# Kernel tuning notes

Hardware: AMD Instinct MI355X
Metric: run time of the kernel (lower is better)

The kernel has to match this reference:

```python
import jax, jax.numpy as jnp
import numpy as np

BINS = 10


def setup_inputs() -> dict:
    key = jax.random.key(0)
    k1, k2 = jax.random.split(key)
    N, C = 4194304, 16
    inputs = jax.random.normal(k1, (N, C), dtype=jnp.float32)
    target = jax.random.randint(k2, (N,), 0, 2, dtype=jnp.int64)
    return {"inputs": inputs, "target": target}


def reference(inputs, target):
    N = inputs.shape[0]
    edges = jnp.arange(BINS + 1, dtype=inputs.dtype) / BINS  # [0, 0.1, ..., 1.0]

    # p_t = softmax(inputs)[i, target_i]
    logp = jax.nn.log_softmax(inputs, axis=1)
    p_t = jnp.take_along_axis(jnp.exp(logp), target[:, None], axis=1)[:, 0]

    # gradient norm g = |p_t - target| (detached in the original)
    g = jnp.abs(jax.lax.stop_gradient(p_t) - target.astype(inputs.dtype))

    # bin index: matches (g >= edges[i]) & (g < edges[i+1]); clip handles g == 1.0
    bin_idx = jnp.clip(jnp.searchsorted(edges, g, side="right") - 1, 0, BINS - 1)

    # per-bin counts via one scatter-add (replaces the per-bin CPU loop)
    counts = jax.ops.segment_sum(jnp.ones_like(g), bin_idx, num_segments=BINS)
    counts = jnp.maximum(counts, 1.0)  # occupied bins always have count >= 1

    # weights[i] = (N / bins) / num_in_bin(i)
    weights = (N / BINS) / counts[bin_idx]

    # weighted cross entropy, summed
    nll = -jnp.take_along_axis(logp, target[:, None], axis=1)[:, 0]
    return jnp.sum(nll * weights)
```

## Files before the change

kernel.cpp:

```cpp
#include <hip/hip_runtime.h>

#define BINS 10

__global__ __launch_bounds__(256) void ghm_main(const float* __restrict__ x,
                                                const int* __restrict__ tgt,
                                                double* __restrict__ g_sum,
                                                unsigned int* __restrict__ g_cnt,
                                                int n_rows) {
    __shared__ double s_sum[BINS];
    __shared__ unsigned int s_cnt[BINS];
    if (threadIdx.x < BINS) { s_sum[threadIdx.x] = 0.0; s_cnt[threadIdx.x] = 0u; }
    __syncthreads();

    const int j = threadIdx.x & 3;
    const int quad = (blockIdx.x * blockDim.x + threadIdx.x) >> 2;
    const int quads_total = (gridDim.x * blockDim.x) >> 2;

    const float edges[BINS + 1] = {0.0f, 0.1f, 0.2f, 0.3f, 0.4f, 0.5f,
                                   0.6f, 0.7f, 0.8f, 0.9f, 1.0f};

    for (int row = quad; row < n_rows; row += quads_total) {
        const float4 v = ((const float4*)x)[row * 4 + j];

        float m = fmaxf(fmaxf(v.x, v.y), fmaxf(v.z, v.w));
        m = fmaxf(m, __shfl_xor(m, 1));
        m = fmaxf(m, __shfl_xor(m, 2));

        float s = expf(v.x - m) + expf(v.y - m) + expf(v.z - m) + expf(v.w - m);
        s += __shfl_xor(s, 1);
        s += __shfl_xor(s, 2);

        if (j == 0) {
            const int t = tgt[row];
            const float xt = (t == 0) ? v.x : ((t == 1) ? v.y : ((t == 2) ? v.z : v.w));
            const float logp = xt - m - logf(s);
            const float p = expf(logp);
            const float g = fabsf(p - (float)t);

            int b = 0;
            #pragma unroll
            for (int k = 1; k <= BINS; ++k) b += (g >= edges[k]) ? 1 : 0;
            if (b > BINS - 1) b = BINS - 1;

            atomicAdd(&s_cnt[b], 1u);
            atomicAdd(&s_sum[b], (double)(-logp));
        }
    }
    __syncthreads();

    if (threadIdx.x < BINS) {
        if (s_cnt[threadIdx.x] != 0u) {
            atomicAdd(&g_cnt[threadIdx.x], s_cnt[threadIdx.x]);
            atomicAdd(&g_sum[threadIdx.x], s_sum[threadIdx.x]);
        }
    }
}

__global__ void ghm_final(const double* __restrict__ g_sum,
                          const unsigned int* __restrict__ g_cnt,
                          float* __restrict__ out, int n_rows) {
    if (threadIdx.x == 0 && blockIdx.x == 0) {
        const double scale = (double)n_rows / (double)BINS;
        double total = 0.0;
        for (int b = 0; b < BINS; ++b) {
            double c = (double)g_cnt[b];
            if (c < 1.0) c = 1.0;
            total += g_sum[b] / c;
        }
        out[0] = (float)(total * scale);
    }
}

extern "C" void kernel_launch(void* const* d_in, const int* in_sizes, int n_in,
                              void* d_out, int out_size, void* d_ws, size_t ws_size,
                              hipStream_t stream) {
    const float* x = (const float*)d_in[0];
    const int* tgt = (const int*)d_in[1];
    const int n_rows = in_sizes[1];

    double* g_sum = (double*)d_ws;
    unsigned int* g_cnt = (unsigned int*)((char*)d_ws + BINS * sizeof(double));

    hipMemsetAsync(d_ws, 0, BINS * (sizeof(double) + sizeof(unsigned int)), stream);

    const int block = 256;
    const int grid = 2048;
    ghm_main<<<grid, block, 0, stream>>>(x, tgt, g_sum, g_cnt, n_rows);
    ghm_final<<<1, 64, 0, stream>>>(g_sum, g_cnt, (float*)d_out, n_rows);
}
```

Measured before the change: 400.1 us.

## Privatize per-thread bin histograms in LDS and reduce per-block partials without atomics

Each thread now processes a whole 16-column row (four float4 loads) instead of four threads sharing a row with shuffles. It accumulates into private per-thread bin slots in padded shared memory, replacing contended shared-memory double and uint atomics. A tree reduction then produces per-block partials written to workspace, and a 64-lane final kernel reduces them, so the memset is no longer needed. The trade-offs are float instead of double per-thread accumulation, a larger LDS footprint, and a smaller grid.

```diff
diff --git a/kernel.cpp b/kernel.cpp
--- a/kernel.cpp
+++ b/kernel.cpp
@@ -1,74 +1,102 @@
 #include <hip/hip_runtime.h>
 
 #define BINS 10
+#define PAD 11
+#define GRID 1024
+#define BLOCK 256
 
-__global__ __launch_bounds__(256) void ghm_main(const float* __restrict__ x,
-                                                const int* __restrict__ tgt,
-                                                double* __restrict__ g_sum,
-                                                unsigned int* __restrict__ g_cnt,
-                                                int n_rows) {
-    __shared__ double s_sum[BINS];
-    __shared__ unsigned int s_cnt[BINS];
-    if (threadIdx.x < BINS) { s_sum[threadIdx.x] = 0.0; s_cnt[threadIdx.x] = 0u; }
-    __syncthreads();
+__global__ __launch_bounds__(BLOCK) void ghm_main(const float* __restrict__ x,
+                                                  const int* __restrict__ tgt,
+                                                  float* __restrict__ p_sum,
+                                                  unsigned int* __restrict__ p_cnt,
+                                                  int n_rows) {
+    __shared__ float s_sum[BLOCK * PAD];
+    __shared__ unsigned int s_cnt[BLOCK * PAD];
 
-    const int j = threadIdx.x & 3;
-    const int quad = (blockIdx.x * blockDim.x + threadIdx.x) >> 2;
-    const int quads_total = (gridDim.x * blockDim.x) >> 2;
+    const int t = threadIdx.x;
+    #pragma unroll
+    for (int b = 0; b < BINS; ++b) { s_sum[t * PAD + b] = 0.0f; s_cnt[t * PAD + b] = 0u; }
 
-    const float edges[BINS + 1] = {0.0f, 0.1f, 0.2f, 0.3f, 0.4f, 0.5f,
-                                   0.6f, 0.7f, 0.8f, 0.9f, 1.0f};
+    const int gid = blockIdx.x * BLOCK + t;
+    const int nthreads = GRID * BLOCK;
+    const float4* __restrict__ xv = (const float4*)x;
 
-    for (int row = quad; row < n_rows; row += quads_total) {
-        const float4 v = ((const float4*)x)[row * 4 + j];
+    const float edges[BINS] = {0.1f, 0.2f, 0.3f, 0.4f, 0.5f,
+                               0.6f, 0.7f, 0.8f, 0.9f, 1.0f};
 
-        float m = fmaxf(fmaxf(v.x, v.y), fmaxf(v.z, v.w));
-        m = fmaxf(m, __shfl_xor(m, 1));
-        m = fmaxf(m, __shfl_xor(m, 2));
+    for (int r = gid; r < n_rows; r += nthreads) {
+        const float4 v0 = xv[(size_t)r * 4 + 0];
+        const float4 v1 = xv[(size_t)r * 4 + 1];
+        const float4 v2 = xv[(size_t)r * 4 + 2];
+        const float4 v3 = xv[(size_t)r * 4 + 3];
+        const int tg = tgt[r];
 
-        float s = expf(v.x - m) + expf(v.y - m) + expf(v.z - m) + expf(v.w - m);
-        s += __shfl_xor(s, 1);
-        s += __shfl_xor(s, 2);
+        float m = fmaxf(fmaxf(fmaxf(v0.x, v0.y), fmaxf(v0.z, v0.w)),
+                        fmaxf(fmaxf(v1.x, v1.y), fmaxf(v1.z, v1.w)));
+        m = fmaxf(m, fmaxf(fmaxf(fmaxf(v2.x, v2.y), fmaxf(v2.z, v2.w)),
+                           fmaxf(fmaxf(v3.x, v3.y), fmaxf(v3.z, v3.w))));
 
-        if (j == 0) {
-            const int t = tgt[row];
-            const float xt = (t == 0) ? v.x : ((t == 1) ? v.y : ((t == 2) ? v.z : v.w));
-            const float logp = xt - m - logf(s);
-            const float p = expf(logp);
-            const float g = fabsf(p - (float)t);
+        float s = expf(v0.x - m) + expf(v0.y - m) + expf(v0.z - m) + expf(v0.w - m)
+                + expf(v1.x - m) + expf(v1.y - m) + expf(v1.z - m) + expf(v1.w - m)
+                + expf(v2.x - m) + expf(v2.y - m) + expf(v2.z - m) + expf(v2.w - m)
+                + expf(v3.x - m) + expf(v3.y - m) + expf(v3.z - m) + expf(v3.w - m);
 
-            int b = 0;
-            #pragma unroll
-            for (int k = 1; k <= BINS; ++k) b += (g >= edges[k]) ? 1 : 0;
-            if (b > BINS - 1) b = BINS - 1;
+        const float4 vs = (tg < 8) ? ((tg < 4) ? v0 : v1) : ((tg < 12) ? v2 : v3);
+        const int c = tg & 3;
+        const float xt = (c < 2) ? ((c == 0) ? vs.x : vs.y) : ((c == 2) ? vs.z : vs.w);
 
-            atomicAdd(&s_cnt[b], 1u);
-            atomicAdd(&s_sum[b], (double)(-logp));
-        }
+        const float logp = xt - m - logf(s);
+        const float g = fabsf(expf(logp) - (float)tg);
+
+        int b = 0;
+        #pragma unroll
+        for (int k = 0; k < BINS; ++k) b += (g >= edges[k]) ? 1 : 0;
+        if (b > BINS - 1) b = BINS - 1;
+
+        s_sum[t * PAD + b] += -logp;
+        s_cnt[t * PAD + b] += 1u;
     }
     __syncthreads();
 
-    if (threadIdx.x < BINS) {
-        if (s_cnt[threadIdx.x] != 0u) {
-            atomicAdd(&g_cnt[threadIdx.x], s_cnt[threadIdx.x]);
-            atomicAdd(&g_sum[threadIdx.x], s_sum[threadIdx.x]);
+    for (int off = BLOCK / 2; off > 0; off >>= 1) {
+        if (t < off) {
+            #pragma unroll
+            for (int b = 0; b < BINS; ++b) {
+                s_sum[t * PAD + b] += s_sum[(t + off) * PAD + b];
+                s_cnt[t * PAD + b] += s_cnt[(t + off) * PAD + b];
+            }
         }
+        __syncthreads();
+    }
+
+    if (t < BINS) {
+        p_sum[t * GRID + blockIdx.x] = s_sum[t];
+        p_cnt[t * GRID + blockIdx.x] = s_cnt[t];
     }
 }
 
-__global__ void ghm_final(const double* __restrict__ g_sum,
-                          const unsigned int* __restrict__ g_cnt,
+__global__ void ghm_final(const float* __restrict__ p_sum,
+                          const unsigned int* __restrict__ p_cnt,
                           float* __restrict__ out, int n_rows) {
-    if (threadIdx.x == 0 && blockIdx.x == 0) {
-        const double scale = (double)n_rows / (double)BINS;
-        double total = 0.0;
-        for (int b = 0; b < BINS; ++b) {
-            double c = (double)g_cnt[b];
-            if (c < 1.0) c = 1.0;
-            total += g_sum[b] / c;
+    const int lane = threadIdx.x;
+    double total = 0.0;
+    for (int b = 0; b < BINS; ++b) {
+        double s = 0.0;
+        unsigned long long c = 0;
+        for (int k = lane; k < GRID; k += 64) {
+            s += (double)p_sum[b * GRID + k];
+            c += (unsigned long long)p_cnt[b * GRID + k];
         }
-        out[0] = (float)(total * scale);
+        #pragma unroll
+        for (int off = 32; off > 0; off >>= 1) {
+            s += __shfl_xor(s, off);
+            c += __shfl_xor(c, off);
+        }
+        double cd = (double)c;
+        if (cd < 1.0) cd = 1.0;
+        total += s / cd;
     }
+    if (lane == 0) out[0] = (float)(total * ((double)n_rows / (double)BINS));
 }
 
 extern "C" void kernel_launch(void* const* d_in, const int* in_sizes, int n_in,
@@ -78,13 +106,9 @@
     const int* tgt = (const int*)d_in[1];
     const int n_rows = in_sizes[1];
 
-    double* g_sum = (double*)d_ws;
-    unsigned int* g_cnt = (unsigned int*)((char*)d_ws + BINS * sizeof(double));
+    float* p_sum = (float*)d_ws;
+    unsigned int* p_cnt = (unsigned int*)((char*)d_ws + BINS * GRID * sizeof(float));
 
-    hipMemsetAsync(d_ws, 0, BINS * (sizeof(double) + sizeof(unsigned int)), stream);
-
-    const int block = 256;
-    const int grid = 2048;
-    ghm_main<<<grid, block, 0, stream>>>(x, tgt, g_sum, g_cnt, n_rows);
-    ghm_final<<<1, 64, 0, stream>>>(g_sum, g_cnt, (float*)d_out, n_rows);
+    ghm_main<<<GRID, BLOCK, 0, stream>>>(x, tgt, p_sum, p_cnt, n_rows);
+    ghm_final<<<1, 64, 0, stream>>>(p_sum, p_cnt, (float*)d_out, n_rows);
 }
```

After: 420.8 us. +5.2%, slower.
